# Performance work log

Measured on AMD Instinct MI355X. Metric: run time of the kernel, lower is better.

## Reference

```python
import jax, jax.numpy as jnp
import numpy as np

B, T, C = 2, 2048, 2048
E, K, S, F = 8, 2, 1, 1408
AUX_COEF, Z_COEF = 0.01, 0.001


def setup_inputs() -> dict:
    key = jax.random.key(0)
    ks = jax.random.split(key, 8)
    sc = 1.0 / np.sqrt(C)
    sf = 1.0 / np.sqrt(F)
    return {
        "x": jax.random.normal(ks[0], (B, T, C), jnp.float32),
        "gate_w": jax.random.normal(ks[1], (E, C), jnp.float32) * sc,   # torch Linear weight [out,in]
        "w1": jax.random.normal(ks[2], (E, F, C), jnp.float32) * sc,    # routed expert up-proj
        "w2": jax.random.normal(ks[3], (E, C, F), jnp.float32) * sf,    # routed expert down-proj
        "sw1": jax.random.normal(ks[4], (S, F, C), jnp.float32) * sc,   # shared expert up-proj
        "sw2": jax.random.normal(ks[5], (S, C, F), jnp.float32) * sf,   # shared expert down-proj
        "alpha": jnp.ones((C,), jnp.float32),                            # HyperConnection scale on MoE out
        "beta": jnp.ones((C,), jnp.float32),                             # HyperConnection scale on residual x
    }


def reference(x, gate_w, w1, w2, sw1, sw2, alpha, beta):
    Bv, Tv, Cv = x.shape
    xf = x.reshape(-1, Cv)                                  # [N, C]
    logits = xf @ gate_w.T                                  # [N, E]
    probs = jax.nn.softmax(logits, axis=-1)
    weights, selected = jax.lax.top_k(probs, K)             # [N, K]
    weights = weights / jnp.sum(weights, axis=-1, keepdims=True)
    aux_loss = AUX_COEF * jnp.sum(jnp.mean(probs, axis=0) ** 2)
    z_loss = Z_COEF * jnp.mean(jax.nn.logsumexp(logits, axis=-1) ** 2)
    # combine[n, e] = routing weight of expert e for token n (0 if not selected)
    combine = jnp.sum(jax.nn.one_hot(selected, E, dtype=xf.dtype) * weights[..., None], axis=1)  # [N, E]
    out = jnp.zeros_like(xf)
    for e in range(E):  # fixed small expert count; weight is 0 for unrouted tokens
        h = jax.nn.silu(xf @ w1[e].T) @ w2[e].T             # [N, C]
        out = out + combine[:, e:e + 1] * h
    for s in range(S):
        out = out + jax.nn.silu(xf @ sw1[s].T) @ sw2[s].T
    y = alpha * out.reshape(Bv, Tv, Cv) + beta * x           # HyperConnection residual mix
    return y, aux_loss + z_loss
```

## Files before the change

### kernel.cpp

```cpp
#include <hip/hip_runtime.h>


#define TOKS 4096
#define CD 2048
#define FD 1408
#define RROWS 8192
#define NTMAX 104

typedef unsigned short u16;
typedef float f32x4 __attribute__((ext_vector_type(4)));
typedef __bf16 bf16x8 __attribute__((ext_vector_type(8)));

__device__ __forceinline__ u16 f2bf(float f) {
  unsigned u = __float_as_uint(f);
  u += 0x7fffu + ((u >> 16) & 1u);
  return (u16)(u >> 16);
}

__global__ __launch_bounds__(256) void gate_kernel(
    const float* __restrict__ x, const float* __restrict__ gw,
    float* __restrict__ combine, float* __restrict__ part, int* __restrict__ sel,
    u16* __restrict__ xb)
{
  const int lane = threadIdx.x & 63;
  const int wave = threadIdx.x >> 6;
  const int n = blockIdx.x * 4 + wave;
  const float* xr = x + (size_t)n * CD;
  u16* xbr = xb + (size_t)n * CD;
  float p[8] = {0,0,0,0,0,0,0,0};
#pragma unroll
  for (int it = 0; it < 8; ++it) {
    const int idx = it * 256 + lane * 4;
    const float4 xv = *(const float4*)(xr + idx);
    ushort4 xo;
    xo.x = f2bf(xv.x); xo.y = f2bf(xv.y); xo.z = f2bf(xv.z); xo.w = f2bf(xv.w);
    *(ushort4*)(xbr + idx) = xo;
#pragma unroll
    for (int e = 0; e < 8; ++e) {
      const float4 gv = *(const float4*)(gw + e * CD + idx);
      p[e] += xv.x * gv.x + xv.y * gv.y + xv.z * gv.z + xv.w * gv.w;
    }
  }
#pragma unroll
  for (int e = 0; e < 8; ++e) {
#pragma unroll
    for (int m = 32; m > 0; m >>= 1) p[e] += __shfl_xor(p[e], m, 64);
  }
  float mx = p[0];
#pragma unroll
  for (int e = 1; e < 8; ++e) mx = fmaxf(mx, p[e]);
  float s = 0.f, pr[8];
#pragma unroll
  for (int e = 0; e < 8; ++e) { pr[e] = __expf(p[e] - mx); s += pr[e]; }
  const float inv = 1.f / s;
#pragma unroll
  for (int e = 0; e < 8; ++e) pr[e] *= inv;
  const float lse = mx + __logf(s);
  int i1 = 0;
#pragma unroll
  for (int e = 1; e < 8; ++e) if (pr[e] > pr[i1]) i1 = e;
  int i2 = (i1 == 0) ? 1 : 0;
#pragma unroll
  for (int e = 0; e < 8; ++e) if (e != i1 && pr[e] > pr[i2]) i2 = e;
  const float rs = 1.f / (pr[i1] + pr[i2]);

  __shared__ float pl[4][12];
  if (lane == 0) {
    float* cr = combine + (size_t)n * 16;
#pragma unroll
    for (int e = 0; e < 8; ++e) cr[e] = 0.f;
    cr[i1] = pr[i1] * rs;
    cr[i2] = pr[i2] * rs;
    cr[8] = 1.0f;
    sel[n] = i1 | (i2 << 4);
#pragma unroll
    for (int e = 0; e < 8; ++e) pl[wave][e] = pr[e];
    pl[wave][8] = lse * lse;
  }
  __syncthreads();
  if (threadIdx.x < 9)
    part[(size_t)blockIdx.x * 16 + threadIdx.x] =
        pl[0][threadIdx.x] + pl[1][threadIdx.x] + pl[2][threadIdx.x] + pl[3][threadIdx.x];
}

__global__ void route_kernel(const int* __restrict__ sel, int* __restrict__ le,
                             int* __restrict__ pos, int* __restrict__ cntoff,
                             int* __restrict__ tileMap)
{
  const int lane = threadIdx.x;
  const unsigned long long lt = (1ull << lane) - 1ull;
  int cnt[8] = {0,0,0,0,0,0,0,0};
  for (int c = 0; c < TOKS / 64; ++c) {
    const int s = sel[c * 64 + lane];
    const int e1 = s & 15, e2 = (s >> 4) & 15;
#pragma unroll
    for (int e = 0; e < 8; ++e)
      cnt[e] += __popcll(__ballot(e1 == e)) + __popcll(__ballot(e2 == e));
  }
  int off[8]; off[0] = 0;
#pragma unroll
  for (int e = 1; e < 8; ++e) off[e] = off[e - 1] + cnt[e - 1];
  int base[8];
#pragma unroll
  for (int e = 0; e < 8; ++e) base[e] = off[e];
  for (int c = 0; c < TOKS / 64; ++c) {
    const int n = c * 64 + lane;
    const int s = sel[n];
    const int e1 = s & 15, e2 = (s >> 4) & 15;
#pragma unroll
    for (int e = 0; e < 8; ++e) {
      const unsigned long long m1 = __ballot(e1 == e);
      const unsigned long long m2 = __ballot(e2 == e);
      if (e1 == e) { const int r = base[e] + __popcll(m1 & lt); le[r] = n; pos[2 * n] = r; }
      if (e2 == e) { const int r = base[e] + __popcll(m1) + __popcll(m2 & lt); le[r] = n; pos[2 * n + 1] = r; }
      base[e] += __popcll(m1) + __popcll(m2);
    }
  }
  if (lane < 8) { cntoff[lane] = cnt[lane]; cntoff[16 + lane] = off[lane]; }
  if (lane == 8) { cntoff[8] = TOKS; cntoff[24] = RROWS; }
  if (lane == 0) {
    int t = 0;
    for (int e = 0; e < 8; ++e)
      for (int m = 0; m < cnt[e]; m += 128) tileMap[t++] = e | (m << 4);
    for (int m = 0; m < TOKS; m += 128) tileMap[t++] = 8 | (m << 4);
    cntoff[25] = t;
  }
}

__global__ void finalize_kernel(const float* __restrict__ part, float* __restrict__ loss_out)
{
  __shared__ float sm[256][10];
  float loc[9] = {0,0,0,0,0,0,0,0,0};
  for (int b = threadIdx.x; b < 1024; b += 256)
#pragma unroll
    for (int c = 0; c < 9; ++c) loc[c] += part[(size_t)b * 16 + c];
#pragma unroll
  for (int c = 0; c < 9; ++c) sm[threadIdx.x][c] = loc[c];
  __syncthreads();
  for (int off = 128; off > 0; off >>= 1) {
    if (threadIdx.x < off)
#pragma unroll
      for (int c = 0; c < 9; ++c) sm[threadIdx.x][c] += sm[threadIdx.x + off][c];
    __syncthreads();
  }
  if (threadIdx.x == 0) {
    float aux = 0.f;
#pragma unroll
    for (int e = 0; e < 8; ++e) { const float m = sm[0][e] * (1.f / TOKS); aux += m * m; }
    const float z = sm[0][8] * (1.f / TOKS);
    loss_out[0] = 0.01f * aux + 0.001f * z;
  }
}

#define W14  5767168
#define SW14 720896
__global__ void cast_all_kernel(const float4* __restrict__ w1, const float4* __restrict__ sw1,
                                const float4* __restrict__ w2, const float4* __restrict__ sw2,
                                u16* __restrict__ w1b, u16* __restrict__ w2b)
{
  const int total = 2 * (W14 + SW14);
  int i = blockIdx.x * blockDim.x + threadIdx.x;
  const int stride = gridDim.x * blockDim.x;
  for (; i < total; i += stride) {
    int j = i;
    const float4* src; u16* dst;
    if (j < W14)                   { src = w1;  dst = w1b; }
    else if ((j -= W14) < SW14)    { src = sw1; dst = w1b + (size_t)8 * FD * CD; }
    else if ((j -= SW14) < W14)    { src = w2;  dst = w2b; }
    else                           { j -= W14; src = sw2; dst = w2b + (size_t)8 * CD * FD; }
    const float4 v = src[j];
    ushort4 o;
    o.x = f2bf(v.x); o.y = f2bf(v.y); o.z = f2bf(v.z); o.w = f2bf(v.w);
    *(ushort4*)(dst + (size_t)j * 4) = o;
  }
}

template<int MODE>
__global__ __launch_bounds__(256, 2) void gemm_bt(
    const u16* __restrict__ Abase, const u16* __restrict__ Bbase,
    u16* __restrict__ outBF, const float* __restrict__ combine,
    const int* __restrict__ le, const int* __restrict__ cntoff,
    const int* __restrict__ tileMap)
{
  constexpr int K   = (MODE == 0) ? CD : FD;
  constexpr int OS  = (MODE == 0) ? FD : CD;
  constexpr int NY  = (MODE == 0) ? 11 : 16;
  constexpr int NKT = K >> 6;
  constexpr int Q   = NTMAX * NY / 8;

  __shared__ __attribute__((aligned(16))) u16 smA[2][128 * 64];
  __shared__ __attribute__((aligned(16))) u16 smB[2][128 * 64];

  const int orig = blockIdx.x + gridDim.x * blockIdx.y;
  const int wgid = (orig & 7) * Q + (orig >> 3);
  const int t = wgid / NY;
  const int y = wgid - t * NY;
  const int NT = cntoff[25];
  if (t >= NT) return;
  const int packed = tileMap[t];
  const int e = packed & 15;
  const int m0 = packed >> 4;
  const int cnt = cntoff[e];
  const int off = cntoff[16 + e];
  const int n0 = y * 128;

  const int tid  = threadIdx.x;
  const int ln   = tid & 63;
  const int wv   = tid >> 6;
  const int wr   = wv >> 1, wc = wv & 1;
  const int la15 = ln & 15;
  const int g16  = ln >> 4;

  const u16* Bp = Bbase + (size_t)e * FD * CD;

  const int srow = ln >> 3;
  const int sgrp = (((ln & 7) ^ srow) << 3);
  const u16* pA[4];
  const u16* pB[4];
#pragma unroll
  for (int c = 0; c < 4; ++c) {
    const int rloc = c * 32 + wv * 8 + srow;
    size_t arow;
    if (MODE == 0)
      arow = (e == 8) ? (size_t)(m0 + rloc)
                      : (size_t)le[min(off + m0 + rloc, RROWS - 1)];
    else
      arow = (size_t)(off + m0 + rloc);
    pA[c] = Abase + arow * K + sgrp;
    pB[c] = Bp + (size_t)(n0 + rloc) * K + sgrp;
  }

#define STAGE(buf, kt)                                                                        \
  {                                                                                           \
    const int kof_ = (kt) << 6;                                                               \
    _Pragma("unroll")                                                                         \
    for (int c_ = 0; c_ < 4; ++c_) {                                                          \
      __builtin_amdgcn_global_load_lds(                                                       \
          (const __attribute__((address_space(1))) void*)(pA[c_] + kof_),                     \
          (__attribute__((address_space(3))) void*)(&smA[buf][c_ * 2048 + wv * 512]),         \
          16, 0, 0);                                                                          \
      __builtin_amdgcn_global_load_lds(                                                       \
          (const __attribute__((address_space(1))) void*)(pB[c_] + kof_),                     \
          (__attribute__((address_space(3))) void*)(&smB[buf][c_ * 2048 + wv * 512]),         \
          16, 0, 0);                                                                          \
    }                                                                                         \
  }

  f32x4 acc[4][4] = {};

  STAGE(0, 0)
  asm volatile("s_waitcnt vmcnt(0)" ::: "memory");
  __builtin_amdgcn_s_barrier();
  asm volatile("" ::: "memory");

#pragma unroll 1
  for (int kt = 0; kt < NKT; ++kt) {
    const int cur = kt & 1;
    if (kt + 1 < NKT) STAGE(cur ^ 1, kt + 1)
    const u16* sa = &smA[cur][0];
    const u16* sb = &smB[cur][0];
#pragma unroll
    for (int kk = 0; kk < 2; ++kk) {
      const int gg = kk * 4 + g16;
      bf16x8 af[4], bv[4];
#pragma unroll
      for (int i = 0; i < 4; ++i) {
        const int r = wr * 64 + i * 16 + la15;
        af[i] = *(const bf16x8*)(sa + r * 64 + (((gg ^ (r & 7))) << 3));
      }
#pragma unroll
      for (int j = 0; j < 4; ++j) {
        const int r = wc * 64 + j * 16 + la15;
        bv[j] = *(const bf16x8*)(sb + r * 64 + (((gg ^ (r & 7))) << 3));
      }
#pragma unroll
      for (int i = 0; i < 4; ++i)
#pragma unroll
        for (int j = 0; j < 4; ++j)
          acc[i][j] = __builtin_amdgcn_mfma_f32_16x16x32_bf16(af[i], bv[j], acc[i][j], 0, 0, 0);
    }
    if (kt + 1 < NKT) {
      asm volatile("s_waitcnt vmcnt(0)" ::: "memory");
      asm volatile("" ::: "memory");
      __builtin_amdgcn_s_barrier();
      asm volatile("" ::: "memory");
    }
  }
#undef STAGE

#pragma unroll
  for (int i = 0; i < 4; ++i) {
    const int rloc0 = wr * 64 + i * 16 + (g16 << 2);
#pragma unroll
    for (int q = 0; q < 4; ++q) {
      const int rloc = rloc0 + q;
      if (m0 + rloc >= cnt) continue;
      float sc = 1.f;
      if (MODE == 0) {
        const int tok = (e == 8) ? (m0 + rloc) : le[off + m0 + rloc];
        sc = combine[(size_t)tok * 16 + e];
      }
#pragma unroll
      for (int j = 0; j < 4; ++j) {
        const int col = n0 + wc * 64 + j * 16 + la15;
        const float v = acc[i][j][q];
        const float h = (MODE == 0) ? (sc * v * (1.f / (1.f + __expf(-v)))) : v;
        outBF[(size_t)(off + m0 + rloc) * OS + col] = f2bf(h);
      }
    }
  }
}

__global__ __launch_bounds__(256) void gather_kernel(
    const u16* __restrict__ Yc, const int* __restrict__ pos,
    const float* __restrict__ x, const float* __restrict__ alpha,
    const float* __restrict__ beta, float* __restrict__ out)
{
  const int n = blockIdx.x;
  const int c0 = threadIdx.x * 8;
  const int p1 = pos[2 * n], p2 = pos[2 * n + 1];
  const bf16x8 a = *(const bf16x8*)(Yc + (size_t)p1 * CD + c0);
  const bf16x8 b = *(const bf16x8*)(Yc + (size_t)p2 * CD + c0);
  const bf16x8 s = *(const bf16x8*)(Yc + ((size_t)RROWS + n) * CD + c0);
  const float* xr = x + (size_t)n * CD + c0;
  float* orow = out + (size_t)n * CD + c0;
#pragma unroll
  for (int j = 0; j < 8; ++j) {
    const float v = (float)a[j] + (float)b[j] + (float)s[j];
    orow[j] = alpha[c0 + j] * v + beta[c0 + j] * xr[j];
  }
}

extern "C" void kernel_launch(void* const* d_in, const int* in_sizes, int n_in,
                              void* d_out, int out_size, void* d_ws, size_t ws_size,
                              hipStream_t stream)
{
  (void)in_sizes; (void)n_in; (void)out_size; (void)ws_size;
  const float* x     = (const float*)d_in[0];
  const float* gw    = (const float*)d_in[1];
  const float* w1    = (const float*)d_in[2];
  const float* w2    = (const float*)d_in[3];
  const float* sw1   = (const float*)d_in[4];
  const float* sw2   = (const float*)d_in[5];
  const float* alpha = (const float*)d_in[6];
  const float* beta  = (const float*)d_in[7];
  float* out = (float*)d_out;

  char* ws = (char*)d_ws;
  float* combine = (float*)(ws + 0);
  float* part    = (float*)(ws + 262144);
  int*   sel     = (int*)(ws + 327680);
  int*   le      = (int*)(ws + 344064);
  int*   pos     = (int*)(ws + 376832);
  int*   cntoff  = (int*)(ws + 409600);
  int*   tileMap = (int*)(ws + 409856);
  u16*   xb      = (u16*)(ws + 410368);
  u16*   w1b     = (u16*)(ws + 17187584);
  u16*   w2b     = (u16*)(ws + 69092096);
  u16*   Hcomp   = (u16*)(ws + 120996608);
  u16*   Ycomp   = (u16*)(ws + 155599616);

  gate_kernel<<<1024, 256, 0, stream>>>(x, gw, combine, part, sel, xb);
  route_kernel<<<1, 64, 0, stream>>>(sel, le, pos, cntoff, tileMap);
  finalize_kernel<<<1, 256, 0, stream>>>(part, out + (size_t)TOKS * CD);
  cast_all_kernel<<<4096, 256, 0, stream>>>((const float4*)w1, (const float4*)sw1,
                                            (const float4*)w2, (const float4*)sw2, w1b, w2b);
  gemm_bt<0><<<dim3(NTMAX, 11), 256, 0, stream>>>(xb, w1b, Hcomp, combine, le, cntoff, tileMap);
  gemm_bt<1><<<dim3(NTMAX, 16), 256, 0, stream>>>(Hcomp, w2b, Ycomp, nullptr, nullptr, cntoff, tileMap);
  gather_kernel<<<TOKS, 256, 0, stream>>>(Ycomp, pos, x, alpha, beta, out);
}
```

Measured before the change: 410.6 us.

## Fuse weight casts into gate and GEMM kernels with persistent atomic tile scheduling

The w1 cast now runs inside the gate kernel over an enlarged grid. The w2 cast is moved into the up-projection GEMM, where persistent workgroups pull work from an atomic counter and take cast chunks once all GEMM tiles are claimed. Both GEMMs become persistent 512-block kernels that replace the old fixed grid with its early exit. The intent is to remove the separate cast kernel pass and overlap the memory-bound cast with compute. The cost is extra atomics and barriers per tile and a loss of the previous XCD-aware tile swizzle.

Measured after the change: 524.1 us. 1.28x slower.

```diff
diff --git a/kernel.cpp b/kernel.cpp
--- a/kernel.cpp
+++ b/kernel.cpp
@@ -5,7 +5,10 @@
 #define CD 2048
 #define FD 1408
 #define RROWS 8192
-#define NTMAX 104
+#define W14 5767168
+#define TOTF4 6488064
+#define CASTCHUNK 32768
+#define NCAST2 198
 
 typedef unsigned short u16;
 typedef float f32x4 __attribute__((ext_vector_type(4)));
@@ -17,70 +20,80 @@
   return (u16)(u >> 16);
 }
 
-__global__ __launch_bounds__(256) void gate_kernel(
+__global__ __launch_bounds__(256) void gatecast_kernel(
     const float* __restrict__ x, const float* __restrict__ gw,
     float* __restrict__ combine, float* __restrict__ part, int* __restrict__ sel,
-    u16* __restrict__ xb)
-{
-  const int lane = threadIdx.x & 63;
-  const int wave = threadIdx.x >> 6;
-  const int n = blockIdx.x * 4 + wave;
-  const float* xr = x + (size_t)n * CD;
-  u16* xbr = xb + (size_t)n * CD;
-  float p[8] = {0,0,0,0,0,0,0,0};
-#pragma unroll
-  for (int it = 0; it < 8; ++it) {
-    const int idx = it * 256 + lane * 4;
-    const float4 xv = *(const float4*)(xr + idx);
-    ushort4 xo;
-    xo.x = f2bf(xv.x); xo.y = f2bf(xv.y); xo.z = f2bf(xv.z); xo.w = f2bf(xv.w);
-    *(ushort4*)(xbr + idx) = xo;
+    u16* __restrict__ xb,
+    const float4* __restrict__ w1, const float4* __restrict__ sw1, u16* __restrict__ w1b)
+{
+  if (blockIdx.x < 1024) {
+    const int lane = threadIdx.x & 63;
+    const int wave = threadIdx.x >> 6;
+    const int n = blockIdx.x * 4 + wave;
+    const float* xr = x + (size_t)n * CD;
+    u16* xbr = xb + (size_t)n * CD;
+    float p[8] = {0,0,0,0,0,0,0,0};
+#pragma unroll
+    for (int it = 0; it < 8; ++it) {
+      const int idx = it * 256 + lane * 4;
+      const float4 xv = *(const float4*)(xr + idx);
+      ushort4 xo;
+      xo.x = f2bf(xv.x); xo.y = f2bf(xv.y); xo.z = f2bf(xv.z); xo.w = f2bf(xv.w);
+      *(ushort4*)(xbr + idx) = xo;
+#pragma unroll
+      for (int e = 0; e < 8; ++e) {
+        const float4 gv = *(const float4*)(gw + e * CD + idx);
+        p[e] += xv.x * gv.x + xv.y * gv.y + xv.z * gv.z + xv.w * gv.w;
+      }
+    }
 #pragma unroll
     for (int e = 0; e < 8; ++e) {
-      const float4 gv = *(const float4*)(gw + e * CD + idx);
-      p[e] += xv.x * gv.x + xv.y * gv.y + xv.z * gv.z + xv.w * gv.w;
-    }
-  }
-#pragma unroll
-  for (int e = 0; e < 8; ++e) {
-#pragma unroll
-    for (int m = 32; m > 0; m >>= 1) p[e] += __shfl_xor(p[e], m, 64);
-  }
-  float mx = p[0];
-#pragma unroll
-  for (int e = 1; e < 8; ++e) mx = fmaxf(mx, p[e]);
-  float s = 0.f, pr[8];
-#pragma unroll
-  for (int e = 0; e < 8; ++e) { pr[e] = __expf(p[e] - mx); s += pr[e]; }
-  const float inv = 1.f / s;
-#pragma unroll
-  for (int e = 0; e < 8; ++e) pr[e] *= inv;
-  const float lse = mx + __logf(s);
-  int i1 = 0;
-#pragma unroll
-  for (int e = 1; e < 8; ++e) if (pr[e] > pr[i1]) i1 = e;
-  int i2 = (i1 == 0) ? 1 : 0;
-#pragma unroll
-  for (int e = 0; e < 8; ++e) if (e != i1 && pr[e] > pr[i2]) i2 = e;
-  const float rs = 1.f / (pr[i1] + pr[i2]);
-
-  __shared__ float pl[4][12];
-  if (lane == 0) {
-    float* cr = combine + (size_t)n * 16;
-#pragma unroll
-    for (int e = 0; e < 8; ++e) cr[e] = 0.f;
-    cr[i1] = pr[i1] * rs;
-    cr[i2] = pr[i2] * rs;
-    cr[8] = 1.0f;
-    sel[n] = i1 | (i2 << 4);
-#pragma unroll
-    for (int e = 0; e < 8; ++e) pl[wave][e] = pr[e];
-    pl[wave][8] = lse * lse;
-  }
-  __syncthreads();
-  if (threadIdx.x < 9)
-    part[(size_t)blockIdx.x * 16 + threadIdx.x] =
-        pl[0][threadIdx.x] + pl[1][threadIdx.x] + pl[2][threadIdx.x] + pl[3][threadIdx.x];
+#pragma unroll
+      for (int m = 32; m > 0; m >>= 1) p[e] += __shfl_xor(p[e], m, 64);
+    }
+    float mx = p[0];
+#pragma unroll
+    for (int e = 1; e < 8; ++e) mx = fmaxf(mx, p[e]);
+    float s = 0.f, pr[8];
+#pragma unroll
+    for (int e = 0; e < 8; ++e) { pr[e] = __expf(p[e] - mx); s += pr[e]; }
+    const float inv = 1.f / s;
+#pragma unroll
+    for (int e = 0; e < 8; ++e) pr[e] *= inv;
+    const float lse = mx + __logf(s);
+    int i1 = 0;
+#pragma unroll
+    for (int e = 1; e < 8; ++e) if (pr[e] > pr[i1]) i1 = e;
+    int i2 = (i1 == 0) ? 1 : 0;
+#pragma unroll
+    for (int e = 0; e < 8; ++e) if (e != i1 && pr[e] > pr[i2]) i2 = e;
+    const float rs = 1.f / (pr[i1] + pr[i2]);
+
+    __shared__ float pl[4][12];
+    if (lane == 0) {
+      float* cr = combine + (size_t)n * 16;
+#pragma unroll
+      for (int e = 0; e < 8; ++e) cr[e] = 0.f;
+      cr[i1] = pr[i1] * rs;
+      cr[i2] = pr[i2] * rs;
+      cr[8] = 1.0f;
+      sel[n] = i1 | (i2 << 4);
+#pragma unroll
+      for (int e = 0; e < 8; ++e) pl[wave][e] = pr[e];
+      pl[wave][8] = lse * lse;
+    }
+    __syncthreads();
+    if (threadIdx.x < 9)
+      part[(size_t)blockIdx.x * 16 + threadIdx.x] =
+          pl[0][threadIdx.x] + pl[1][threadIdx.x] + pl[2][threadIdx.x] + pl[3][threadIdx.x];
+  }
+  const int stride = gridDim.x * blockDim.x;
+  for (int j = blockIdx.x * blockDim.x + threadIdx.x; j < TOTF4; j += stride) {
+    const float4 v = (j < W14) ? w1[j] : sw1[j - W14];
+    ushort4 o;
+    o.x = f2bf(v.x); o.y = f2bf(v.y); o.z = f2bf(v.z); o.w = f2bf(v.w);
+    *(ushort4*)(w1b + (size_t)j * 4) = o;
+  }
 }
 
 __global__ void route_kernel(const int* __restrict__ sel, int* __restrict__ le,
@@ -118,6 +131,7 @@
   }
   if (lane < 8) { cntoff[lane] = cnt[lane]; cntoff[16 + lane] = off[lane]; }
   if (lane == 8) { cntoff[8] = TOKS; cntoff[24] = RROWS; }
+  if (lane == 9) { cntoff[26] = 0; cntoff[27] = 0; }
   if (lane == 0) {
     int t = 0;
     for (int e = 0; e < 8; ++e)
@@ -152,57 +166,22 @@
   }
 }
 
-#define W14  5767168
-#define SW14 720896
-__global__ void cast_all_kernel(const float4* __restrict__ w1, const float4* __restrict__ sw1,
-                                const float4* __restrict__ w2, const float4* __restrict__ sw2,
-                                u16* __restrict__ w1b, u16* __restrict__ w2b)
-{
-  const int total = 2 * (W14 + SW14);
-  int i = blockIdx.x * blockDim.x + threadIdx.x;
-  const int stride = gridDim.x * blockDim.x;
-  for (; i < total; i += stride) {
-    int j = i;
-    const float4* src; u16* dst;
-    if (j < W14)                   { src = w1;  dst = w1b; }
-    else if ((j -= W14) < SW14)    { src = sw1; dst = w1b + (size_t)8 * FD * CD; }
-    else if ((j -= SW14) < W14)    { src = w2;  dst = w2b; }
-    else                           { j -= W14; src = sw2; dst = w2b + (size_t)8 * CD * FD; }
-    const float4 v = src[j];
-    ushort4 o;
-    o.x = f2bf(v.x); o.y = f2bf(v.y); o.z = f2bf(v.z); o.w = f2bf(v.w);
-    *(ushort4*)(dst + (size_t)j * 4) = o;
-  }
-}
-
 template<int MODE>
 __global__ __launch_bounds__(256, 2) void gemm_bt(
     const u16* __restrict__ Abase, const u16* __restrict__ Bbase,
     u16* __restrict__ outBF, const float* __restrict__ combine,
-    const int* __restrict__ le, const int* __restrict__ cntoff,
-    const int* __restrict__ tileMap)
+    const int* __restrict__ le, int* __restrict__ cntoff,
+    const int* __restrict__ tileMap,
+    const float4* __restrict__ c2a, const float4* __restrict__ c2b, u16* __restrict__ c2dst)
 {
   constexpr int K   = (MODE == 0) ? CD : FD;
   constexpr int OS  = (MODE == 0) ? FD : CD;
   constexpr int NY  = (MODE == 0) ? 11 : 16;
   constexpr int NKT = K >> 6;
-  constexpr int Q   = NTMAX * NY / 8;
 
   __shared__ __attribute__((aligned(16))) u16 smA[2][128 * 64];
   __shared__ __attribute__((aligned(16))) u16 smB[2][128 * 64];
-
-  const int orig = blockIdx.x + gridDim.x * blockIdx.y;
-  const int wgid = (orig & 7) * Q + (orig >> 3);
-  const int t = wgid / NY;
-  const int y = wgid - t * NY;
-  const int NT = cntoff[25];
-  if (t >= NT) return;
-  const int packed = tileMap[t];
-  const int e = packed & 15;
-  const int m0 = packed >> 4;
-  const int cnt = cntoff[e];
-  const int off = cntoff[16 + e];
-  const int n0 = y * 128;
+  __shared__ int sh_i;
 
   const int tid  = threadIdx.x;
   const int ln   = tid & 63;
@@ -210,25 +189,8 @@
   const int wr   = wv >> 1, wc = wv & 1;
   const int la15 = ln & 15;
   const int g16  = ln >> 4;
-
-  const u16* Bp = Bbase + (size_t)e * FD * CD;
-
   const int srow = ln >> 3;
   const int sgrp = (((ln & 7) ^ srow) << 3);
-  const u16* pA[4];
-  const u16* pB[4];
-#pragma unroll
-  for (int c = 0; c < 4; ++c) {
-    const int rloc = c * 32 + wv * 8 + srow;
-    size_t arow;
-    if (MODE == 0)
-      arow = (e == 8) ? (size_t)(m0 + rloc)
-                      : (size_t)le[min(off + m0 + rloc, RROWS - 1)];
-    else
-      arow = (size_t)(off + m0 + rloc);
-    pA[c] = Abase + arow * K + sgrp;
-    pB[c] = Bp + (size_t)(n0 + rloc) * K + sgrp;
-  }
 
 #define STAGE(buf, kt)                                                                        \
   {                                                                                           \
@@ -246,69 +208,116 @@
     }                                                                                         \
   }
 
-  f32x4 acc[4][4] = {};
-
-  STAGE(0, 0)
-  asm volatile("s_waitcnt vmcnt(0)" ::: "memory");
-  __builtin_amdgcn_s_barrier();
-  asm volatile("" ::: "memory");
+  for (;;) {
+    __syncthreads();
+    if (tid == 0) sh_i = atomicAdd(&cntoff[26 + MODE], 1);
+    __syncthreads();
+    const int i = sh_i;
+    const int ntile = cntoff[25] * NY;
+    if (i >= ntile) {
+      if (MODE == 1) break;
+      const int c = i - ntile;
+      if (c >= NCAST2) break;
+      const int cbase = c * CASTCHUNK;
+      for (int k = tid; k < CASTCHUNK; k += 256) {
+        const int j = cbase + k;
+        const float4 v = (j < W14) ? c2a[j] : c2b[j - W14];
+        ushort4 o;
+        o.x = f2bf(v.x); o.y = f2bf(v.y); o.z = f2bf(v.z); o.w = f2bf(v.w);
+        *(ushort4*)(c2dst + (size_t)j * 4) = o;
+      }
+      continue;
+    }
+
+    const int t = i / NY;
+    const int y = i - t * NY;
+    const int packed = tileMap[t];
+    const int e = packed & 15;
+    const int m0 = packed >> 4;
+    const int cnt = cntoff[e];
+    const int off = cntoff[16 + e];
+    const int n0 = y * 128;
+    const u16* Bp = Bbase + (size_t)e * FD * CD;
+
+    const u16* pA[4];
+    const u16* pB[4];
+#pragma unroll
+    for (int c = 0; c < 4; ++c) {
+      const int rloc = c * 32 + wv * 8 + srow;
+      size_t arow;
+      if (MODE == 0)
+        arow = (e == 8) ? (size_t)(m0 + rloc)
+                        : (size_t)le[min(off + m0 + rloc, RROWS - 1)];
+      else
+        arow = (size_t)(off + m0 + rloc);
+      pA[c] = Abase + arow * K + sgrp;
+      pB[c] = Bp + (size_t)(n0 + rloc) * K + sgrp;
+    }
+
+    f32x4 acc[4][4] = {};
+
+    STAGE(0, 0)
+    asm volatile("s_waitcnt vmcnt(0)" ::: "memory");
+    __builtin_amdgcn_s_barrier();
+    asm volatile("" ::: "memory");
 
 #pragma unroll 1
-  for (int kt = 0; kt < NKT; ++kt) {
-    const int cur = kt & 1;
-    if (kt + 1 < NKT) STAGE(cur ^ 1, kt + 1)
-    const u16* sa = &smA[cur][0];
-    const u16* sb = &smB[cur][0];
-#pragma unroll
-    for (int kk = 0; kk < 2; ++kk) {
-      const int gg = kk * 4 + g16;
-      bf16x8 af[4], bv[4];
-#pragma unroll
-      for (int i = 0; i < 4; ++i) {
-        const int r = wr * 64 + i * 16 + la15;
-        af[i] = *(const bf16x8*)(sa + r * 64 + (((gg ^ (r & 7))) << 3));
-      }
-#pragma unroll
-      for (int j = 0; j < 4; ++j) {
-        const int r = wc * 64 + j * 16 + la15;
-        bv[j] = *(const bf16x8*)(sb + r * 64 + (((gg ^ (r & 7))) << 3));
-      }
-#pragma unroll
-      for (int i = 0; i < 4; ++i)
-#pragma unroll
-        for (int j = 0; j < 4; ++j)
-          acc[i][j] = __builtin_amdgcn_mfma_f32_16x16x32_bf16(af[i], bv[j], acc[i][j], 0, 0, 0);
-    }
-    if (kt + 1 < NKT) {
-      asm volatile("s_waitcnt vmcnt(0)" ::: "memory");
-      asm volatile("" ::: "memory");
-      __builtin_amdgcn_s_barrier();
-      asm volatile("" ::: "memory");
+    for (int kt = 0; kt < NKT; ++kt) {
+      const int cur = kt & 1;
+      if (kt + 1 < NKT) STAGE(cur ^ 1, kt + 1)
+      const u16* sa = &smA[cur][0];
+      const u16* sb = &smB[cur][0];
+#pragma unroll
+      for (int kk = 0; kk < 2; ++kk) {
+        const int gg = kk * 4 + g16;
+        bf16x8 af[4], bv[4];
+#pragma unroll
+        for (int ii = 0; ii < 4; ++ii) {
+          const int r = wr * 64 + ii * 16 + la15;
+          af[ii] = *(const bf16x8*)(sa + r * 64 + (((gg ^ (r & 7))) << 3));
+        }
+#pragma unroll
+        for (int j = 0; j < 4; ++j) {
+          const int r = wc * 64 + j * 16 + la15;
+          bv[j] = *(const bf16x8*)(sb + r * 64 + (((gg ^ (r & 7))) << 3));
+        }
+#pragma unroll
+        for (int ii = 0; ii < 4; ++ii)
+#pragma unroll
+          for (int j = 0; j < 4; ++j)
+            acc[ii][j] = __builtin_amdgcn_mfma_f32_16x16x32_bf16(af[ii], bv[j], acc[ii][j], 0, 0, 0);
+      }
+      if (kt + 1 < NKT) {
+        asm volatile("s_waitcnt vmcnt(0)" ::: "memory");
+        asm volatile("" ::: "memory");
+        __builtin_amdgcn_s_barrier();
+        asm volatile("" ::: "memory");
+      }
+    }
+
+#pragma unroll
+    for (int ii = 0; ii < 4; ++ii) {
+      const int rloc0 = wr * 64 + ii * 16 + (g16 << 2);
+#pragma unroll
+      for (int q = 0; q < 4; ++q) {
+        const int rloc = rloc0 + q;
+        if (m0 + rloc >= cnt) continue;
+        float sc = 1.f;
+        if (MODE == 0) {
+          const int tok = (e == 8) ? (m0 + rloc) : le[off + m0 + rloc];
+          sc = combine[(size_t)tok * 16 + e];
+        }
+#pragma unroll
+        for (int j = 0; j < 4; ++j) {
+          const int col = n0 + wc * 64 + j * 16 + la15;
+          const float v = acc[ii][j][q];
+          const float h = (MODE == 0) ? (sc * v * (1.f / (1.f + __expf(-v)))) : v;
+          outBF[(size_t)(off + m0 + rloc) * OS + col] = f2bf(h);
+        }
+      }
     }
   }
 #undef STAGE
-
-#pragma unroll
-  for (int i = 0; i < 4; ++i) {
-    const int rloc0 = wr * 64 + i * 16 + (g16 << 2);
-#pragma unroll
-    for (int q = 0; q < 4; ++q) {
-      const int rloc = rloc0 + q;
-      if (m0 + rloc >= cnt) continue;
-      float sc = 1.f;
-      if (MODE == 0) {
-        const int tok = (e == 8) ? (m0 + rloc) : le[off + m0 + rloc];
-        sc = combine[(size_t)tok * 16 + e];
-      }
-#pragma unroll
-      for (int j = 0; j < 4; ++j) {
-        const int col = n0 + wc * 64 + j * 16 + la15;
-        const float v = acc[i][j][q];
-        const float h = (MODE == 0) ? (sc * v * (1.f / (1.f + __expf(-v)))) : v;
-        outBF[(size_t)(off + m0 + rloc) * OS + col] = f2bf(h);
-      }
-    }
-  }
 }
 
 __global__ __launch_bounds__(256) void gather_kernel(
@@ -360,12 +369,13 @@
   u16*   Hcomp   = (u16*)(ws + 120996608);
   u16*   Ycomp   = (u16*)(ws + 155599616);
 
-  gate_kernel<<<1024, 256, 0, stream>>>(x, gw, combine, part, sel, xb);
+  gatecast_kernel<<<2048, 256, 0, stream>>>(x, gw, combine, part, sel, xb,
+                                            (const float4*)w1, (const float4*)sw1, w1b);
   route_kernel<<<1, 64, 0, stream>>>(sel, le, pos, cntoff, tileMap);
   finalize_kernel<<<1, 256, 0, stream>>>(part, out + (size_t)TOKS * CD);
-  cast_all_kernel<<<4096, 256, 0, stream>>>((const float4*)w1, (const float4*)sw1,
-                                            (const float4*)w2, (const float4*)sw2, w1b, w2b);
-  gemm_bt<0><<<dim3(NTMAX, 11), 256, 0, stream>>>(xb, w1b, Hcomp, combine, le, cntoff, tileMap);
-  gemm_bt<1><<<dim3(NTMAX, 16), 256, 0, stream>>>(Hcomp, w2b, Ycomp, nullptr, nullptr, cntoff, tileMap);
+  gemm_bt<0><<<512, 256, 0, stream>>>(xb, w1b, Hcomp, combine, le, cntoff, tileMap,
+                                      (const float4*)w2, (const float4*)sw2, w2b);
+  gemm_bt<1><<<512, 256, 0, stream>>>(Hcomp, w2b, Ycomp, nullptr, le, cntoff, tileMap,
+                                      nullptr, nullptr, nullptr);
   gather_kernel<<<TOKS, 256, 0, stream>>>(Ycomp, pos, x, alpha, beta, out);
 }
```
